# Performance work log

Measured on AMD Instinct MI355X. Metric: run time of the kernel, lower is better.

Reference implementation:

```python
import jax, jax.numpy as jnp
import numpy as np

HEADS = 8


def setup_inputs() -> dict:
    key = jax.random.key(0)
    ks = jax.random.split(key, 6)
    dim = 256
    s = 0.02
    return {
        "x": jax.random.normal(ks[0], (8, dim, 32, 32), jnp.float32),
        "w_qkv": jax.random.normal(ks[1], (3 * dim, dim), jnp.float32) * s,
        "w_out": jax.random.normal(ks[2], (dim, dim), jnp.float32) * s,
        "b_out": jnp.zeros((dim,), jnp.float32),
        "w_g1": jax.random.normal(ks[3], (dim // 4, dim), jnp.float32) * s,
        "b_g1": jnp.zeros((dim // 4,), jnp.float32),
        "w_g2": jax.random.normal(ks[4], (1, dim // 4), jnp.float32) * s,
        "b_g2": jnp.zeros((1,), jnp.float32),
    }


def _conv1x1(t, w, bias=None):
    # 1x1 conv == channel matmul
    y = jnp.einsum('bchw,oc->bohw', t, w)
    if bias is not None:
        y = y + bias[None, :, None, None]
    return y


def _forward(x, w_qkv, w_out, b_out, w_g1, b_g1, w_g2, b_g2):
    b, c, h, w = x.shape
    heads = HEADS
    d = c // heads
    n = h * w
    m = min(h, w)
    scale = d ** (-0.5)

    qkv = _conv1x1(x, w_qkv)  # [b, 3c, h, w]

    def to_heads(t):  # 'b (h d) x y -> b h (x y) d'
        return t.reshape(b, heads, d, n).transpose(0, 1, 3, 2)

    q, k, v = (to_heads(t) for t in jnp.split(qkv, 3, axis=1))

    attn = jax.nn.softmax(jnp.einsum('bhid,bhjd->bhij', q, k) * scale, axis=-1)

    # diagonal branch (anti-diagonal scores are computed in the original but
    # never used in the output -> omitted as dead code)
    q2d = q.reshape(b, heads, h, w, d)
    k2d = k.reshape(b, heads, h, w, d)
    q_dm = jnp.diagonal(q2d, axis1=2, axis2=3)  # [b, heads, d, m]
    k_dm = jnp.diagonal(k2d, axis1=2, axis2=3)
    diag_main = jnp.einsum('bhnd,bhmd->bhnm', q_dm, k_dm) * scale  # [b, heads, d, d]
    diag_vec = jnp.diagonal(diag_main.mean(axis=1), axis1=-2, axis2=-1)  # [b, d]
    diag_vec = jnp.pad(diag_vec, ((0, 0), (0, n - m)))  # [b, n] (d == m)

    DIAG_WEIGHT = 0.3
    enhanced = attn + DIAG_WEIGHT * diag_vec[:, None, :, None]

    out = jnp.einsum('bhij,bhjd->bhid', enhanced, v)  # [b, heads, n, d]
    out = out.reshape(b, heads, h, w, d).transpose(0, 1, 4, 2, 3).reshape(b, c, h, w)

    # left/right asymmetry gate
    mid = w // 2
    left = x[:, :, :, :mid]
    right = x[:, :, :, mid:]
    asym = jnp.abs(left - right[:, :, :, ::-1])  # [b, c, h, w/2]
    # adaptive_avg_pool2d (h, w/2) -> (h, w) with even w == width repeat by 2
    pooled = jnp.repeat(asym, 2, axis=3)
    g = _conv1x1(pooled, w_g1, b_g1)
    g = jax.nn.gelu(g, approximate=False)
    g = jax.nn.sigmoid(_conv1x1(g, w_g2, b_g2))  # [b, 1, h, w]

    out = out * (1.0 + g)
    return _conv1x1(out, w_out, b_out)


def reference(x, w_qkv, w_out, b_out, w_g1, b_g1, w_g2, b_g2):
    return _forward(x, w_qkv, w_out, b_out, w_g1, b_g1, w_g2, b_g2)
```

## Files before the change

### kernel.cpp

```cpp
#include <hip/hip_runtime.h>
#include <hip/hip_bf16.h>
#include <math.h>

#define B 8
#define C 256
#define HEADS 8
#define D 32
#define NPIX 1024
#define OC 768
#define SCALE 0.17677669529663687f
#define LOG2E 1.4426950408889634f

typedef unsigned int uint;
typedef unsigned short u16;
typedef __attribute__((ext_vector_type(8))) short bf16x8;
typedef __attribute__((ext_vector_type(4))) short bf16x4;
typedef __attribute__((ext_vector_type(4))) float f32x4;

static __device__ inline u16 f2bf(float f) {
  uint u = __float_as_uint(f);
  return (u16)((u + 0x7fffu + ((u >> 16) & 1u)) >> 16);
}
static __device__ inline float bfval(u16 v) { return __uint_as_float((uint)v << 16); }
static __device__ inline float bf_lo(uint u) { return __uint_as_float(u << 16); }
static __device__ inline float bf_hi(uint u) { return __uint_as_float(u & 0xffff0000u); }

static __device__ inline uint pk2(float lo, float hi) {
  union { __hip_bfloat162 h; uint u; } cv;
  cv.h = __float22bfloat162_rn(float2{lo, hi});
  return cv.u;
}

__global__ __launch_bounds__(256) void k_prep_gate(
    const float* __restrict__ x, const float* __restrict__ wqkv,
    const float* __restrict__ wout,
    const float* __restrict__ wg1, const float* __restrict__ bg1,
    const float* __restrict__ wg2, const float* __restrict__ bg2,
    u16* __restrict__ WQ, u16* __restrict__ WO, u16* __restrict__ XT,
    float* __restrict__ gate) {
  const int bid = blockIdx.x, t = threadIdx.x;
  __shared__ float smem[16 * 257 + 16 * 65];
  if (bid < 256) {
    const float* src;
    u16* dst;
    int base;
    if (bid < 192) { src = wqkv; dst = WQ; base = bid * 1024; }
    else           { src = wout; dst = WO; base = (bid - 192) * 1024; }
    float4 v = *(const float4*)(src + base + t * 4);
    uint2 pk = make_uint2((uint)f2bf(v.x) | ((uint)f2bf(v.y) << 16),
                          (uint)f2bf(v.z) | ((uint)f2bf(v.w) << 16));
    *(uint2*)(dst + base + t * 4) = pk;
    return;
  }
  if (bid < 768) {
    u16 (*tile)[65] = (u16(*)[65])smem;
    const int id = bid - 256;
    const int pt = id & 15, ct = (id >> 4) & 3, b = id >> 6;
    {
      const int px = t & 63, cq = t >> 6;
      const float* xb = x + ((size_t)(b * C + ct * 64)) * NPIX + pt * 64;
#pragma unroll
      for (int m = 0; m < 16; ++m) {
        const int c = cq * 16 + m;
        tile[c][px] = f2bf(xb[(size_t)c * NPIX + px]);
      }
    }
    __syncthreads();
    {
      const int cc = t & 63, pq = t >> 6;
      const int c = ct * 64 + cc;
      const int kc = c >> 5, quad = (c >> 3) & 3, mm = c & 7;
      u16* dst = XT + ((size_t)((b * 64 + pt * 4 + pq) * 8 + kc) * 512 +
                       quad * 128 + mm);
#pragma unroll
      for (int m = 0; m < 16; ++m)
        dst[m * 8] = tile[cc][pq * 16 + m];
    }
    return;
  }
  const int id = bid - 768;
  const int h = id & 31, b = id >> 5;
  float* pl = smem;
  float* gl = smem + 16 * 257;
  {
    const int c = t;
    const float* row = x + ((size_t)(b * C + c) * NPIX + h * 32);
    float v[32];
#pragma unroll
    for (int m = 0; m < 32; ++m) v[m] = row[m];
#pragma unroll
    for (int k = 0; k < 16; ++k) pl[k * 257 + c] = fabsf(v[k] - v[31 - k]);
  }
  __syncthreads();

  const int o16 = t >> 4, k = t & 15;
#pragma unroll 1
  for (int p = 0; p < 4; ++p) {
    const int o = p * 16 + o16;
    const float* wr = wg1 + o * C;
    float a0 = 0.f, a1 = 0.f, a2 = 0.f, a3 = 0.f;
#pragma unroll 4
    for (int c = 0; c < C; c += 4) {
      a0 += wr[c]     * pl[k * 257 + c];
      a1 += wr[c + 1] * pl[k * 257 + c + 1];
      a2 += wr[c + 2] * pl[k * 257 + c + 2];
      a3 += wr[c + 3] * pl[k * 257 + c + 3];
    }
    float a = bg1[o] + ((a0 + a1) + (a2 + a3));
    gl[k * 65 + o] = 0.5f * a * (1.f + erff(a * 0.70710678118654752f));
  }
  __syncthreads();

  if (t < 16) {
    float s = bg2[0];
    for (int o = 0; o < 64; ++o)
      s += wg2[o] * gl[t * 65 + o];
    gate[(b * 32 + h) * 16 + t] = 1.f / (1.f + expf(-s));
  }
}

__global__ __launch_bounds__(256) void k_qkv_mfma(
    const u16* __restrict__ XTF, const u16* __restrict__ WQ,
    u16* __restrict__ Q, u16* __restrict__ Kk, u16* __restrict__ VT) {
  const int ob = blockIdx.x, pb = blockIdx.y, b = blockIdx.z;
  const int t = threadIdx.x;
  const int wv = t >> 6, lane = t & 63;
  const int quad = lane >> 4, l15 = lane & 15;
  const int part = ob >> 2;
  const int odl = (ob & 3) * 64 + wv * 16;
  const int hh = odl >> 5, d0 = odl & 31;
  const int bh = b * HEADS + hh;
  const int pix0 = pb * 128;

  __shared__ u16 sb[2][4096];

  const u16* arow = WQ + (size_t)(ob * 64 + wv * 16 + l15) * C;
  bf16x8 af[8];
#pragma unroll
  for (int kc = 0; kc < 8; ++kc)
    af[kc] = *(const bf16x8*)(arow + kc * 32 + quad * 8);

  const u16* xb = XTF + (size_t)(b * 64 + pb * 8) * 8 * 512;
  const int snt = t >> 5, si = (t & 31) * 16;

  f32x4 acc[8];
#pragma unroll
  for (int nt = 0; nt < 8; ++nt) acc[nt] = (f32x4){0.f, 0.f, 0.f, 0.f};

  {
    const u16* p = xb + (size_t)(snt * 8 + 0) * 512 + si;
    uint4 r0 = *(const uint4*)(p);
    uint4 r1 = *(const uint4*)(p + 8);
    u16* d = &sb[0][snt * 512 + si];
    *(uint4*)(d) = r0;
    *(uint4*)(d + 8) = r1;
  }
  __syncthreads();

  int cur = 0;
  for (int kc = 0; kc < 8; ++kc) {
    uint4 r0, r1;
    if (kc < 7) {
      const u16* p = xb + (size_t)(snt * 8 + kc + 1) * 512 + si;
      r0 = *(const uint4*)(p);
      r1 = *(const uint4*)(p + 8);
    }
    const u16* s = &sb[cur][0];
#pragma unroll
    for (int nt = 0; nt < 8; ++nt) {
      bf16x8 bfr = *(const bf16x8*)(s + nt * 512 + lane * 8);
      acc[nt] = __builtin_amdgcn_mfma_f32_16x16x32_bf16(af[kc], bfr, acc[nt], 0, 0, 0);
    }
    if (kc < 7) {
      u16* d = &sb[cur ^ 1][snt * 512 + si];
      *(uint4*)(d) = r0;
      *(uint4*)(d + 8) = r1;
    }
    __syncthreads();
    cur ^= 1;
  }

  if (part == 0) {
    const float qs = SCALE * LOG2E;
    u16* dst = Q + (size_t)bh * NPIX * D;
#pragma unroll
    for (int nt = 0; nt < 8; ++nt) {
      const int pix = pix0 + nt * 16 + l15;
      uint2 pk = make_uint2(
          (uint)f2bf(acc[nt][0] * qs) | ((uint)f2bf(acc[nt][1] * qs) << 16),
          (uint)f2bf(acc[nt][2] * qs) | ((uint)f2bf(acc[nt][3] * qs) << 16));
      *(uint2*)(dst + (size_t)pix * D + d0 + 4 * quad) = pk;
    }
  } else if (part == 1) {
    u16* kfb = Kk + (size_t)bh * NPIX * D;
    const int lane_k8 = (((d0 >> 3) + (quad >> 1)) * 16 + l15) * 8 + (quad & 1) * 4;
#pragma unroll
    for (int nt = 0; nt < 8; ++nt) {
      uint2 pk = make_uint2(
          (uint)f2bf(acc[nt][0]) | ((uint)f2bf(acc[nt][1]) << 16),
          (uint)f2bf(acc[nt][2]) | ((uint)f2bf(acc[nt][3]) << 16));
      *(uint2*)(kfb + (size_t)(pb * 8 + nt) * 512 + lane_k8) = pk;
    }
  } else {
    u16* vb = VT + (size_t)bh * NPIX * D;
#pragma unroll
    for (int nt = 0; nt < 8; ++nt) {
      const int pix = pix0 + nt * 16 + l15;
      const int jb16 = pix >> 4, qa = (pix >> 2) & 3, m = pix & 3;
#pragma unroll
      for (int r = 0; r < 4; ++r) {
        const int d = d0 + 4 * quad + r;
        const int nta = d >> 4, l15a = d & 15;
        vb[((size_t)(jb16 * 2 + nta) * 64 + qa * 16 + l15a) * 4 + m] =
            f2bf(acc[nt][r]);
      }
    }
  }
}

__global__ __launch_bounds__(256) void k_red(
    const u16* __restrict__ Q, const u16* __restrict__ KF,
    const u16* __restrict__ VT, float* __restrict__ diagv,
    float* __restrict__ colsum) {
  const int bid = blockIdx.x, tid = threadIdx.x;
  __shared__ float red[256];
  if (bid < 8) {
    const int b = bid;
    const int hh = tid >> 5, dd = tid & 31;
    const u16* qb = Q + (size_t)(b * HEADS + hh) * NPIX * D;
    const u16* kb = KF + (size_t)(b * HEADS + hh) * NPIX * D;
    float s = 0.f;
#pragma unroll 4
    for (int t = 0; t < 32; ++t) {
      const int j = t * 33;
      float qv = bfval(qb[(size_t)j * D + dd]);
      float kv = bfval(kb[(size_t)(j >> 4) * 512 +
                          ((dd >> 3) * 16 + (j & 15)) * 8 + (dd & 7)]);
      s += qv * kv;
    }
    red[tid] = s;
    __syncthreads();
    if (tid < 32) {
      float v = 0.f;
#pragma unroll
      for (int h8 = 0; h8 < 8; ++h8) v += red[h8 * 32 + tid];
      diagv[b * 32 + tid] = v * (0.125f / LOG2E);
    }
  } else {
    const int bh = bid - 8;
    const int d = tid >> 3, sl = tid & 7;
    const int nta = d >> 4, l15a = d & 15;
    const u16* vb = VT + (size_t)bh * NPIX * D;
    float s = 0.f;
    for (int jb = 0; jb < 8; ++jb) {
      const int jb16 = sl * 8 + jb;
#pragma unroll
      for (int qa = 0; qa < 4; ++qa) {
        const uint2 u = *(const uint2*)(
            vb + ((size_t)(jb16 * 2 + nta) * 64 + qa * 16 + l15a) * 4);
        s += bf_lo(u.x) + bf_hi(u.x) + bf_lo(u.y) + bf_hi(u.y);
      }
    }
    red[tid] = s;
    __syncthreads();
    if (tid < 32) {
      float v = 0.f;
#pragma unroll
      for (int g = 0; g < 8; ++g) v += red[tid * 8 + g];
      colsum[bh * D + tid] = v;
    }
  }
}

__global__ __launch_bounds__(512, 4) void k_attn(
    const u16* __restrict__ Q, const u16* __restrict__ KF,
    const u16* __restrict__ VF, const float* __restrict__ diagv,
    const float* __restrict__ colsum, u16* __restrict__ AOT) {
  const int qc = blockIdx.x;
  const int bh = blockIdx.y;
  const int b = bh >> 3, hh = bh & 7;
  const int wv = threadIdx.x >> 6, lane = threadIdx.x & 63;
  const int quad = lane >> 4, l15 = lane & 15;
  const int i0 = qc * 128 + wv * 16;

  __shared__ u16 sbuf[2][8192];

  const u16* Qb  = Q  + (size_t)bh * NPIX * D;
  const u16* KFb = KF + (size_t)bh * NPIX * D;
  const u16* VFb = VF + (size_t)bh * NPIX * D;

  bf16x8 qfrag = *(const bf16x8*)(Qb + (size_t)(i0 + l15) * D + quad * 8);

  f32x4 oacc[2];
  oacc[0] = (f32x4){0.f, 0.f, 0.f, 0.f};
  oacc[1] = (f32x4){0.f, 0.f, 0.f, 0.f};
  float lacc[4] = {};

  const int soff = (wv >= 4 ? 4096 : 0) + (wv & 3) * 1024 + lane * 16;
  const u16* gsrc = (wv < 4 ? KFb : VFb) + (wv & 3) * 1024 + lane * 16;

  {
    uint4 a0 = *(const uint4*)(gsrc);
    uint4 a1 = *(const uint4*)(gsrc + 8);
    *(uint4*)(&sbuf[0][soff]) = a0;
    *(uint4*)(&sbuf[0][soff + 8]) = a1;
  }
  __syncthreads();

  int cur = 0;
  for (int it = 0; it < 8; ++it) {
    uint4 p0, p1;
    if (it < 7) {
      const u16* g = gsrc + (size_t)(it + 1) * 4096;
      p0 = *(const uint4*)(g);
      p1 = *(const uint4*)(g + 8);
    }
    const u16* base = cur ? &sbuf[1][0] : &sbuf[0][0];

#pragma unroll
    for (int h2 = 0; h2 < 2; ++h2) {
      const u16* sK = base + h2 * 2048;
      const u16* sV = base + 4096 + h2 * 2048;

      f32x4 st[4];
#pragma unroll
      for (int jt = 0; jt < 4; ++jt) {
        bf16x8 kfrag = *(const bf16x8*)(sK + jt * 512 + lane * 8);
        st[jt] = __builtin_amdgcn_mfma_f32_16x16x32_bf16(
            kfrag, qfrag, (f32x4){0.f, 0.f, 0.f, 0.f}, 0, 0, 0);
      }

#pragma unroll
      for (int jt = 0; jt < 4; ++jt)
#pragma unroll
        for (int r = 0; r < 4; ++r) {
          float pv = exp2f(fminf(st[jt][r], 80.f));
          lacc[r] += pv;
          st[jt][r] = pv;
        }

      __builtin_amdgcn_s_setprio(1);
#pragma unroll
      for (int jt = 0; jt < 4; ++jt) {
        union { uint u[2]; bf16x4 v; } pa;
        pa.u[0] = pk2(st[jt][0], st[jt][1]);
        pa.u[1] = pk2(st[jt][2], st[jt][3]);
#pragma unroll
        for (int nt = 0; nt < 2; ++nt) {
          bf16x4 vfr = *(const bf16x4*)(sV + (jt * 2 + nt) * 256 + lane * 4);
          oacc[nt] = __builtin_amdgcn_mfma_f32_16x16x16bf16_1k(
              pa.v, vfr, oacc[nt], 0, 0, 0);
        }
      }
      __builtin_amdgcn_s_setprio(0);
    }

    if (it < 7) {
      u16* d = cur ? &sbuf[0][soff] : &sbuf[1][soff];
      *(uint4*)(d) = p0;
      *(uint4*)(d + 8) = p1;
    }
    __syncthreads();
    cur ^= 1;
  }

  float lt = (lacc[0] + lacc[1]) + (lacc[2] + lacc[3]);
  lt += __shfl_xor(lt, 16, 64);
  lt += __shfl_xor(lt, 32, 64);
  const float linv = 1.f / lt;
  float rinv[4];
#pragma unroll
  for (int r = 0; r < 4; ++r) rinv[r] = __shfl(linv, quad * 4 + r, 64);

  const bool do_diag = (i0 < 32);
  const int p16 = i0 >> 4;
  u16* aobase = AOT + ((size_t)(b * 64 + p16) * 8 + hh) * 512 + (l15 & 7);
  const int hi8 = l15 >> 3;
#pragma unroll
  for (int nt = 0; nt < 2; ++nt) {
    const int qa = nt * 2 + hi8;
    float cs = do_diag ? colsum[bh * D + (nt * 16 + l15)] : 0.f;
#pragma unroll
    for (int r = 0; r < 4; ++r) {
      const int irow = i0 + quad * 4 + r;
      float o = oacc[nt][r] * rinv[r];
      if (do_diag) o += 0.3f * diagv[b * 32 + irow] * cs;
      aobase[(qa * 16 + quad * 4 + r) * 8] = f2bf(o);
    }
  }
}

__global__ __launch_bounds__(256) void k_out_mfma(
    const u16* __restrict__ AOF, const u16* __restrict__ WO,
    const float* __restrict__ bout, const float* __restrict__ gate,
    float* __restrict__ out) {
  const int ob = blockIdx.x, pb = blockIdx.y, b = blockIdx.z;
  const int t = threadIdx.x;
  const int wv = t >> 6, lane = t & 63;
  const int quad = lane >> 4, l15 = lane & 15;
  const int o0 = ob * 64 + wv * 16;
  const int pix0 = pb * 128;

  __shared__ u16 sb[2][4096];

  const u16* arow = WO + (size_t)(o0 + l15) * C;
  bf16x8 af[8];
#pragma unroll
  for (int kc = 0; kc < 8; ++kc)
    af[kc] = *(const bf16x8*)(arow + kc * 32 + quad * 8);

  const u16* ab = AOF + (size_t)(b * 64 + pb * 8) * 8 * 512;
  const int snt = t >> 5, si = (t & 31) * 16;

  f32x4 acc[8];
#pragma unroll
  for (int nt = 0; nt < 8; ++nt) acc[nt] = (f32x4){0.f, 0.f, 0.f, 0.f};

  {
    const u16* p = ab + (size_t)(snt * 8 + 0) * 512 + si;
    uint4 r0 = *(const uint4*)(p);
    uint4 r1 = *(const uint4*)(p + 8);
    u16* d = &sb[0][snt * 512 + si];
    *(uint4*)(d) = r0;
    *(uint4*)(d + 8) = r1;
  }
  __syncthreads();

  int cur = 0;
  for (int kc = 0; kc < 8; ++kc) {
    uint4 r0, r1;
    if (kc < 7) {
      const u16* p = ab + (size_t)(snt * 8 + kc + 1) * 512 + si;
      r0 = *(const uint4*)(p);
      r1 = *(const uint4*)(p + 8);
    }
    const u16* s = &sb[cur][0];
#pragma unroll
    for (int nt = 0; nt < 8; ++nt) {
      bf16x8 bfr = *(const bf16x8*)(s + nt * 512 + lane * 8);
      acc[nt] = __builtin_amdgcn_mfma_f32_16x16x32_bf16(af[kc], bfr, acc[nt], 0, 0, 0);
    }
    if (kc < 7) {
      u16* d = &sb[cur ^ 1][snt * 512 + si];
      *(uint4*)(d) = r0;
      *(uint4*)(d + 8) = r1;
    }
    __syncthreads();
    cur ^= 1;
  }

#pragma unroll
  for (int nt = 0; nt < 8; ++nt) {
    const int pix = pix0 + nt * 16 + l15;
    const float gf = 1.f + gate[(b * 32 + (pix >> 5)) * 16 + ((pix & 31) >> 1)];
#pragma unroll
    for (int r = 0; r < 4; ++r) {
      const int o = o0 + 4 * quad + r;
      out[((size_t)b * C + o) * NPIX + pix] = acc[nt][r] * gf + bout[o];
    }
  }
}

extern "C" void kernel_launch(void* const* d_in, const int* in_sizes, int n_in,
                              void* d_out, int out_size, void* d_ws, size_t ws_size,
                              hipStream_t stream) {
  const float* x    = (const float*)d_in[0];
  const float* wqkv = (const float*)d_in[1];
  const float* wout = (const float*)d_in[2];
  const float* bout = (const float*)d_in[3];
  const float* wg1  = (const float*)d_in[4];
  const float* bg1  = (const float*)d_in[5];
  const float* wg2  = (const float*)d_in[6];
  const float* bg2  = (const float*)d_in[7];
  float* out = (float*)d_out;

  const size_t SZ = (size_t)B * HEADS * NPIX * D;
  u16* XT = (u16*)d_ws;
  u16* WQ = XT + SZ;
  u16* WO = WQ + (size_t)OC * C;
  u16* Q  = WO + (size_t)C * C;
  u16* Kq = Q + SZ;
  u16* VT = Kq + SZ;
  float* DIAG = (float*)(VT + SZ);
  float* COL  = DIAG + 256;
  float* GATE = COL + 2048;
  u16* AOT = XT;

  hipLaunchKernelGGL(k_prep_gate, dim3(1024), dim3(256), 0, stream,
                     x, wqkv, wout, wg1, bg1, wg2, bg2, WQ, WO, XT, GATE);
  hipLaunchKernelGGL(k_qkv_mfma, dim3(12, 8, B), dim3(256), 0, stream,
                     XT, WQ, Q, Kq, VT);
  hipLaunchKernelGGL(k_red, dim3(72), dim3(256), 0, stream,
                     Q, Kq, VT, DIAG, COL);
  hipLaunchKernelGGL(k_attn, dim3(8, 64), dim3(512), 0, stream,
                     Q, Kq, VT, DIAG, COL, AOT);
  hipLaunchKernelGGL(k_out_mfma, dim3(4, 8, B), dim3(256), 0, stream,
                     AOT, WO, bout, GATE, out);
}
```

Measured before the change: 144.8 us.

## Fuse V column sums into QKV epilogue and vectorize X transpose stores

The per-head column sums of V are now accumulated in the QKV GEMM epilogue with shuffle reductions and atomics, with the buffer zeroed in the prep kernel. This removes the 64 column-sum blocks from the reduction kernel, which now launches only 8 blocks for the diagonal term. The X transpose in the prep kernel is rewritten so each thread packs 8 bf16 values and writes them as one 16-byte store instead of 16 scattered 2-byte stores. The atomics make the float summation order nondeterministic.

```diff
diff --git a/kernel.cpp b/kernel.cpp
--- a/kernel.cpp
+++ b/kernel.cpp
@@ -37,7 +37,7 @@
     const float* __restrict__ wg1, const float* __restrict__ bg1,
     const float* __restrict__ wg2, const float* __restrict__ bg2,
     u16* __restrict__ WQ, u16* __restrict__ WO, u16* __restrict__ XT,
-    float* __restrict__ gate) {
+    float* __restrict__ gate, float* __restrict__ colsum) {
   const int bid = blockIdx.x, t = threadIdx.x;
   __shared__ float smem[16 * 257 + 16 * 65];
   if (bid < 256) {
@@ -50,6 +50,11 @@
     uint2 pk = make_uint2((uint)f2bf(v.x) | ((uint)f2bf(v.y) << 16),
                           (uint)f2bf(v.z) | ((uint)f2bf(v.w) << 16));
     *(uint2*)(dst + base + t * 4) = pk;
+    if (bid == 0) {
+      float4 z = {0.f, 0.f, 0.f, 0.f};
+      *(float4*)(colsum + t * 8) = z;
+      *(float4*)(colsum + t * 8 + 4) = z;
+    }
     return;
   }
   if (bid < 768) {
@@ -67,14 +72,20 @@
     }
     __syncthreads();
     {
-      const int cc = t & 63, pq = t >> 6;
-      const int c = ct * 64 + cc;
-      const int kc = c >> 5, quad = (c >> 3) & 3, mm = c & 7;
-      u16* dst = XT + ((size_t)((b * 64 + pt * 4 + pq) * 8 + kc) * 512 +
-                       quad * 128 + mm);
-#pragma unroll
-      for (int m = 0; m < 16; ++m)
-        dst[m * 8] = tile[cc][pq * 16 + m];
+#pragma unroll
+      for (int uu = 0; uu < 2; ++uu) {
+        const int u = t + uu * 256;
+        const int kc2 = u >> 8, quad = (u >> 6) & 3;
+        const int pq = (u >> 4) & 3, m = u & 15;
+        const int px = pq * 16 + m;
+        union { uint4 w; u16 h[8]; } pk;
+#pragma unroll
+        for (int mm = 0; mm < 8; ++mm)
+          pk.h[mm] = tile[kc2 * 32 + quad * 8 + mm][px];
+        u16* dst = XT + ((size_t)((b * 64 + pt * 4 + pq) * 8 + ct * 2 + kc2) * 512 +
+                         quad * 128 + m * 8);
+        *(uint4*)dst = pk.w;
+      }
     }
     return;
   }
@@ -121,7 +132,8 @@
 
 __global__ __launch_bounds__(256) void k_qkv_mfma(
     const u16* __restrict__ XTF, const u16* __restrict__ WQ,
-    u16* __restrict__ Q, u16* __restrict__ Kk, u16* __restrict__ VT) {
+    u16* __restrict__ Q, u16* __restrict__ Kk, u16* __restrict__ VT,
+    float* __restrict__ colsum) {
   const int ob = blockIdx.x, pb = blockIdx.y, b = blockIdx.z;
   const int t = threadIdx.x;
   const int wv = t >> 6, lane = t & 63;
@@ -203,6 +215,7 @@
     }
   } else {
     u16* vb = VT + (size_t)bh * NPIX * D;
+    float cs[4] = {};
 #pragma unroll
     for (int nt = 0; nt < 8; ++nt) {
       const int pix = pix0 + nt * 16 + l15;
@@ -211,64 +224,50 @@
       for (int r = 0; r < 4; ++r) {
         const int d = d0 + 4 * quad + r;
         const int nta = d >> 4, l15a = d & 15;
-        vb[((size_t)(jb16 * 2 + nta) * 64 + qa * 16 + l15a) * 4 + m] =
-            f2bf(acc[nt][r]);
+        const u16 hv = f2bf(acc[nt][r]);
+        vb[((size_t)(jb16 * 2 + nta) * 64 + qa * 16 + l15a) * 4 + m] = hv;
+        cs[r] += bfval(hv);
       }
+    }
+#pragma unroll
+    for (int r = 0; r < 4; ++r) {
+      cs[r] += __shfl_xor(cs[r], 1, 16);
+      cs[r] += __shfl_xor(cs[r], 2, 16);
+      cs[r] += __shfl_xor(cs[r], 4, 16);
+      cs[r] += __shfl_xor(cs[r], 8, 16);
+    }
+    if (l15 == 0) {
+#pragma unroll
+      for (int r = 0; r < 4; ++r)
+        atomicAdd(&colsum[bh * D + d0 + 4 * quad + r], cs[r]);
     }
   }
 }
 
 __global__ __launch_bounds__(256) void k_red(
     const u16* __restrict__ Q, const u16* __restrict__ KF,
-    const u16* __restrict__ VT, float* __restrict__ diagv,
-    float* __restrict__ colsum) {
-  const int bid = blockIdx.x, tid = threadIdx.x;
+    float* __restrict__ diagv) {
+  const int b = blockIdx.x, tid = threadIdx.x;
   __shared__ float red[256];
-  if (bid < 8) {
-    const int b = bid;
-    const int hh = tid >> 5, dd = tid & 31;
-    const u16* qb = Q + (size_t)(b * HEADS + hh) * NPIX * D;
-    const u16* kb = KF + (size_t)(b * HEADS + hh) * NPIX * D;
-    float s = 0.f;
+  const int hh = tid >> 5, dd = tid & 31;
+  const u16* qb = Q + (size_t)(b * HEADS + hh) * NPIX * D;
+  const u16* kb = KF + (size_t)(b * HEADS + hh) * NPIX * D;
+  float s = 0.f;
 #pragma unroll 4
-    for (int t = 0; t < 32; ++t) {
-      const int j = t * 33;
-      float qv = bfval(qb[(size_t)j * D + dd]);
-      float kv = bfval(kb[(size_t)(j >> 4) * 512 +
-                          ((dd >> 3) * 16 + (j & 15)) * 8 + (dd & 7)]);
-      s += qv * kv;
-    }
-    red[tid] = s;
-    __syncthreads();
-    if (tid < 32) {
-      float v = 0.f;
-#pragma unroll
-      for (int h8 = 0; h8 < 8; ++h8) v += red[h8 * 32 + tid];
-      diagv[b * 32 + tid] = v * (0.125f / LOG2E);
-    }
-  } else {
-    const int bh = bid - 8;
-    const int d = tid >> 3, sl = tid & 7;
-    const int nta = d >> 4, l15a = d & 15;
-    const u16* vb = VT + (size_t)bh * NPIX * D;
-    float s = 0.f;
-    for (int jb = 0; jb < 8; ++jb) {
-      const int jb16 = sl * 8 + jb;
-#pragma unroll
-      for (int qa = 0; qa < 4; ++qa) {
-        const uint2 u = *(const uint2*)(
-            vb + ((size_t)(jb16 * 2 + nta) * 64 + qa * 16 + l15a) * 4);
-        s += bf_lo(u.x) + bf_hi(u.x) + bf_lo(u.y) + bf_hi(u.y);
-      }
-    }
-    red[tid] = s;
-    __syncthreads();
-    if (tid < 32) {
-      float v = 0.f;
-#pragma unroll
-      for (int g = 0; g < 8; ++g) v += red[tid * 8 + g];
-      colsum[bh * D + tid] = v;
-    }
+  for (int t = 0; t < 32; ++t) {
+    const int j = t * 33;
+    float qv = bfval(qb[(size_t)j * D + dd]);
+    float kv = bfval(kb[(size_t)(j >> 4) * 512 +
+                        ((dd >> 3) * 16 + (j & 15)) * 8 + (dd & 7)]);
+    s += qv * kv;
+  }
+  red[tid] = s;
+  __syncthreads();
+  if (tid < 32) {
+    float v = 0.f;
+#pragma unroll
+    for (int h8 = 0; h8 < 8; ++h8) v += red[h8 * 32 + tid];
+    diagv[b * 32 + tid] = v * (0.125f / LOG2E);
   }
 }
 
@@ -487,11 +486,11 @@
   u16* AOT = XT;
 
   hipLaunchKernelGGL(k_prep_gate, dim3(1024), dim3(256), 0, stream,
-                     x, wqkv, wout, wg1, bg1, wg2, bg2, WQ, WO, XT, GATE);
+                     x, wqkv, wout, wg1, bg1, wg2, bg2, WQ, WO, XT, GATE, COL);
   hipLaunchKernelGGL(k_qkv_mfma, dim3(12, 8, B), dim3(256), 0, stream,
-                     XT, WQ, Q, Kq, VT);
-  hipLaunchKernelGGL(k_red, dim3(72), dim3(256), 0, stream,
-                     Q, Kq, VT, DIAG, COL);
+                     XT, WQ, Q, Kq, VT, COL);
+  hipLaunchKernelGGL(k_red, dim3(8), dim3(256), 0, stream,
+                     Q, Kq, DIAG);
   hipLaunchKernelGGL(k_attn, dim3(8, 64), dim3(512), 0, stream,
                      Q, Kq, VT, DIAG, COL, AOT);
   hipLaunchKernelGGL(k_out_mfma, dim3(4, 8, B), dim3(256), 0, stream,
```

After: 144.1 us. No clear change (-0.5%).
